# Optimization experiments

Hardware: AMD Instinct MI355X
Metric: run time of the kernel (lower is better)

## Reference

```python
import jax, jax.numpy as jnp
import numpy as np

B = 2          # point-cloud batches
N_PER_B = 8192 # non-empty pillars per batch
C = 128        # channels
H = 4          # heads
K = 4096       # max_tokens (top-k cap)
LN_EPS = 1e-5


def setup_inputs() -> dict:
    key = jax.random.key(0)
    ks = jax.random.split(key, 6)
    N = B * N_PER_B
    feats = jax.random.normal(ks[0], (N, C), dtype=jnp.float32)
    # equal-sized contiguous batch groups (sorted batch ids)
    batch_idx = jnp.repeat(jnp.arange(B, dtype=jnp.int64), N_PER_B)
    in_proj_w = jax.random.normal(ks[1], (3 * C, C), dtype=jnp.float32) * 0.02
    in_proj_b = jax.random.normal(ks[2], (3 * C,), dtype=jnp.float32) * 0.02
    out_proj_w = jax.random.normal(ks[3], (C, C), dtype=jnp.float32) * 0.02
    out_proj_b = jax.random.normal(ks[4], (C,), dtype=jnp.float32) * 0.02
    ln_w = jnp.ones((C,), dtype=jnp.float32)
    ln_b = jnp.zeros((C,), dtype=jnp.float32)
    return {"feats": feats, "batch_idx": batch_idx, "in_proj_w": in_proj_w,
            "in_proj_b": in_proj_b, "out_proj_w": out_proj_w,
            "out_proj_b": out_proj_b, "ln_w": ln_w, "ln_b": ln_b}


def _sparse_pillar_attn(feats, in_proj_w, in_proj_b, out_proj_w, out_proj_b, ln_w, ln_b):
    Dh = C // H
    x = feats.reshape(B, N_PER_B, C)
    # top-K tokens per batch by L2 feature norm (cap at max_tokens)
    norms = jnp.linalg.norm(x, axis=-1)                      # [B, n]
    _, topk = jax.lax.top_k(norms, K)                        # [B, K]
    xa = jnp.take_along_axis(x, topk[..., None], axis=1)     # [B, K, C]
    # MultiheadAttention (batch_first, self-attn)
    qkv = xa @ in_proj_w.T + in_proj_b                       # [B, K, 3C]
    q, k, v = jnp.split(qkv, 3, axis=-1)
    def heads(t):  # [B, K, C] -> [B, H, K, Dh]
        return t.reshape(B, K, H, Dh).transpose(0, 2, 1, 3)
    q, k, v = heads(q), heads(k), heads(v)
    scores = jnp.einsum('bhqd,bhkd->bhqk', q, k) / jnp.sqrt(jnp.float32(Dh))
    attn = jax.nn.softmax(scores, axis=-1)
    o = jnp.einsum('bhqk,bhkd->bhqd', attn, v)               # [B, H, K, Dh]
    o = o.transpose(0, 2, 1, 3).reshape(B, K, C)
    o = o @ out_proj_w.T + out_proj_b
    # residual + LayerNorm (dropout p=0 -> identity)
    h = xa + o
    mu = jnp.mean(h, axis=-1, keepdims=True)
    var = jnp.mean(jnp.square(h - mu), axis=-1, keepdims=True)
    y = (h - mu) / jnp.sqrt(var + LN_EPS) * ln_w + ln_b      # [B, K, C]
    # scatter back; non-selected tokens unchanged
    gidx = (jnp.arange(B)[:, None] * N_PER_B + topk).reshape(-1)
    return feats.at[gidx].set(y.reshape(-1, C))


def reference(feats, batch_idx, in_proj_w, in_proj_b, out_proj_w, out_proj_b, ln_w, ln_b):
    # batch_idx is sorted with equal group sizes, so groups are contiguous
    return _sparse_pillar_attn(feats, in_proj_w, in_proj_b, out_proj_w, out_proj_b, ln_w, ln_b)
```

## Files before the change

kernel.cpp:

```cpp
#include <hip/hip_runtime.h>
#include <hip/hip_bf16.h>
#include <stdint.h>

#define NPB 8192
#define CB 2
#define CC 128
#define HH 4
#define KTOK 4096
#define DH 32
#define NTOK (CB*KTOK)
#define K2C 0.25503402f

typedef __attribute__((ext_vector_type(8))) short sh8;
typedef __attribute__((ext_vector_type(4))) float fx4;
typedef __attribute__((ext_vector_type(16))) float fx16;
typedef __attribute__((ext_vector_type(2))) uint32_t ux2;
typedef __attribute__((ext_vector_type(4))) uint32_t ux4;

__device__ inline uint16_t f2bf(float f){
  uint32_t x = __float_as_uint(f);
  return (uint16_t)((x + 0x7FFFu + ((x>>16)&1u)) >> 16);
}
__device__ inline uint32_t pk2(float a, float b){
  return (uint32_t)f2bf(a) | ((uint32_t)f2bf(b) << 16);
}
__device__ inline float fast_exp2(float x){
#if __has_builtin(__builtin_amdgcn_exp2f)
  return __builtin_amdgcn_exp2f(x);
#else
  return exp2f(x);
#endif
}
__device__ inline uint32_t cvtpk1(float a, float b){
  uint32_t u;
  asm("v_cvt_pk_bf16_f32 %0, %1, %2" : "=v"(u) : "v"(a), "v"(b));
  return u;
}
__device__ inline void plswap(uint32_t& a, uint32_t& b){
#if __has_builtin(__builtin_amdgcn_permlane32_swap)
  typedef __attribute__((ext_vector_type(2))) unsigned int u2;
  u2 r = __builtin_amdgcn_permlane32_swap(a, b, false, false);
  a = r.x; b = r.y;
#else
  int hi = (threadIdx.x & 63) >> 5;
  uint32_t t = __shfl_xor(hi ? a : b, 32);
  uint32_t na = hi ? t : a;
  uint32_t nb = hi ? b : t;
  a = na; b = nb;
#endif
}
__device__ inline fx4 mfma32(sh8 a, sh8 b, fx4 c){
  return __builtin_amdgcn_mfma_f32_16x16x32_bf16(a, b, c, 0, 0, 0);
}
__device__ inline fx16 mfma32x32(sh8 a, sh8 b, fx16 c){
  return __builtin_amdgcn_mfma_f32_32x32x16_bf16(a, b, c, 0, 0, 0);
}
__device__ inline void gload_lds(const uint16_t* g, uint16_t* l){
  __builtin_amdgcn_global_load_lds(
      (const __attribute__((address_space(1))) uint32_t*)g,
      (__attribute__((address_space(3))) uint32_t*)l,
      16, 0, 0);
}

__global__ __launch_bounds__(256) void k_cpnw(const float* __restrict__ feats,
                                              float* __restrict__ out,
                                              uint32_t* __restrict__ keys,
                                              const float* __restrict__ wq,
                                              const float* __restrict__ wo,
                                              uint16_t* __restrict__ wqb,
                                              uint16_t* __restrict__ wob){
  int bx = blockIdx.x;
  if (bx < 1024){
    int wv = threadIdx.x >> 6, lane = threadIdx.x & 63;
    int row0 = bx*16 + wv*4;
#pragma unroll
    for (int r = 0; r < 4; ++r){
      int row = row0 + r;
      float2 v = *(const float2*)(feats + row*CC + lane*2);
      *(float2*)(out + row*CC + lane*2) = v;
      float s = v.x*v.x + v.y*v.y;
      for (int m = 1; m < 64; m <<= 1) s += __shfl_xor(s, m);
      if (lane == 0) keys[row] = __float_as_uint(s);
    }
  } else {
    int i = (bx - 1024)*256 + threadIdx.x;
    if (i < 3*CC*CC) wqb[i] = f2bf(wq[i]);
    else { int j = i - 3*CC*CC; wob[j] = f2bf(wo[j]); }
  }
}

__global__ __launch_bounds__(1024) void k_select(const uint32_t* __restrict__ keys,
                                                 int* __restrict__ sel){
  __shared__ uint32_t ka[NPB];
  __shared__ uint32_t hist[16*257];
  __shared__ uint32_t sh_prefix, sh_r;
  __shared__ int wsum[17];
  int tid = threadIdx.x, batch = blockIdx.x;
  int wv16 = tid >> 6;
  for (int i = tid; i < NPB; i += 1024) ka[i] = keys[batch*NPB + i];
  if (tid == 0){ sh_prefix = 0u; sh_r = KTOK; }
  __syncthreads();
  for (int pass = 0; pass < 4; ++pass){
    int shift = 24 - 8*pass;
    for (int i = tid; i < 16*257; i += 1024) hist[i] = 0u;
    __syncthreads();
    uint32_t pref = sh_prefix;
    uint32_t r0   = sh_r;
    uint32_t mask = (pass == 0) ? 0u : (0xFFFFFFFFu << (shift + 8));
    uint32_t* myh = &hist[wv16*257];
    for (int e = 0; e < 8; ++e){
      uint32_t k = ka[tid*8 + e];
      if ((k & mask) == pref) atomicAdd(&myh[(k >> shift) & 255], 1u);
    }
    __syncthreads();
    if (tid < 64){
      int lane = tid;
      uint32_t h0v = 0, h1v = 0, h2v = 0, h3v = 0;
      int b0 = lane*4;
#pragma unroll
      for (int w = 0; w < 16; ++w){
        const uint32_t* hw = &hist[w*257 + b0];
        h0v += hw[0]; h1v += hw[1]; h2v += hw[2]; h3v += hw[3];
      }
      uint32_t s3 = h3v, s2 = h2v + s3, s1 = h1v + s2, s0 = h0v + s1;
      uint32_t incl = s0;
      for (int d = 1; d < 64; d <<= 1){
        uint32_t t = __shfl_down(incl, d);
        if (lane + d < 64) incl += t;
      }
      uint32_t exA = incl - s0;
      uint32_t sfx[4] = {s0, s1, s2, s3};
      uint32_t hh[4]  = {h0v, h1v, h2v, h3v};
#pragma unroll
      for (int k = 0; k < 4; ++k){
        uint32_t inc_b = exA + sfx[k];
        uint32_t Sx    = inc_b - hh[k];
        if (Sx < r0 && inc_b >= r0){
          sh_prefix = pref | ((uint32_t)(b0 + k) << shift);
          sh_r = r0 - Sx;
        }
      }
    }
    __syncthreads();
  }
  uint32_t T = sh_prefix; int need = (int)sh_r;
  int lgt = 0, leq = 0;
  for (int e = 0; e < 8; ++e){
    uint32_t k = ka[tid*8 + e];
    lgt += (k > T); leq += (k == T);
  }
  int lane = tid & 63, wv = tid >> 6;
  int egt, tgt, eeq;
  {
    __syncthreads();
    int incl = lgt;
    for (int d = 1; d < 64; d <<= 1){ int t = __shfl_up(incl, d); if (lane >= d) incl += t; }
    if (lane == 63) wsum[wv] = incl;
    __syncthreads();
    if (tid == 0){ int run = 0; for (int w = 0; w < 16; ++w){ int t = wsum[w]; wsum[w] = run; run += t; } wsum[16] = run; }
    __syncthreads();
    egt = wsum[wv] + incl - lgt; tgt = wsum[16];
  }
  {
    __syncthreads();
    int incl = leq;
    for (int d = 1; d < 64; d <<= 1){ int t = __shfl_up(incl, d); if (lane >= d) incl += t; }
    if (lane == 63) wsum[wv] = incl;
    __syncthreads();
    if (tid == 0){ int run = 0; for (int w = 0; w < 16; ++w){ int t = wsum[w]; wsum[w] = run; run += t; } }
    __syncthreads();
    eeq = wsum[wv] + incl - leq;
  }
  int chi = tgt, gpos = egt, epos = eeq;
  for (int e = 0; e < 8; ++e){
    int i = tid*8 + e;
    uint32_t k = ka[i];
    if (k > T){ sel[batch*KTOK + (gpos++)] = batch*NPB + i; }
    else if (k == T){ if (epos < need) sel[batch*KTOK + chi + epos] = batch*NPB + i; epos++; }
  }
}

__global__ __launch_bounds__(256) void k_qkv(const float* __restrict__ feats,
                                             const int* __restrict__ sel,
                                             const uint16_t* __restrict__ wqb,
                                             const float* __restrict__ bias,
                                             uint16_t* __restrict__ Qg,
                                             uint16_t* __restrict__ Kg,
                                             uint16_t* __restrict__ Vt){
  int wave = threadIdx.x >> 6, lane = threadIdx.x & 63;
  int l15 = lane & 15, g = lane >> 4;
  int rt = blockIdx.x;
  int arow = rt*16 + l15;
  int grow = sel[arow];
  sh8 aF[4];
#pragma unroll
  for (int kk = 0; kk < 4; ++kk){
    const float* src = feats + grow*CC + kk*32 + g*8;
    float4 v0 = *(const float4*)(src);
    float4 v1 = *(const float4*)(src + 4);
    ux4 u;
    u.x = cvtpk1(v0.x, v0.y);
    u.y = cvtpk1(v0.z, v0.w);
    u.z = cvtpk1(v1.x, v1.y);
    u.w = cvtpk1(v1.z, v1.w);
    aF[kk] = *(sh8*)&u;
  }
  int tbase = rt*16;
  int b  = tbase >> 12;
  int q0 = (tbase & 4095) + g*4;
#pragma unroll
  for (int cg = 0; cg < 6; ++cg){
    int bcol = (cg*4 + wave)*16 + l15;
    fx4 acc = {0.f,0.f,0.f,0.f};
#pragma unroll
    for (int kk = 0; kk < 4; ++kk){
      sh8 bF = *(const sh8*)(wqb + bcol*CC + kk*32 + g*8);
      acc = mfma32(aF[kk], bF, acc);
    }
    int j = bcol;
    float bj = bias[j];
    if (j < CC){
      int h = j >> 5, d = j & 31;
      uint16_t* p = Qg + ((b*HH + h)*KTOK + q0)*DH + d;
#pragma unroll
      for (int i = 0; i < 4; ++i) p[i*DH] = f2bf((acc[i] + bj) * K2C);
    } else if (j < 2*CC){
      int jj = j - CC; int h = jj >> 5, d = jj & 31;
      uint16_t* p = Kg + ((b*HH + h)*KTOK + q0)*DH + d;
#pragma unroll
      for (int i = 0; i < 4; ++i) p[i*DH] = f2bf(acc[i] + bj);
    } else {
      int jj = j - 2*CC; int h = jj >> 5, d = jj & 31;
      uint16_t* p = Vt + ((b*HH + h)*DH + d)*KTOK + q0;
      ux2 w; w.x = pk2(acc[0]+bj, acc[1]+bj); w.y = pk2(acc[2]+bj, acc[3]+bj);
      *(ux2*)p = w;
    }
  }
}

__global__ __launch_bounds__(1024) void k_attn(const uint16_t* __restrict__ Qg,
                                               const uint16_t* __restrict__ Kg,
                                               const uint16_t* __restrict__ Vtg,
                                               uint16_t* __restrict__ O){
  __shared__ __align__(16) char lds[68096];
  int tid = threadIdx.x;
  int wv = tid >> 6, lane = tid & 63;
  int l31 = lane & 31, hi = lane >> 5;
  int seg = wv & 3, tq = wv >> 2;
  int bh = blockIdx.y;
  int qt = blockIdx.x;
  const uint16_t* Qp = Qg  + bh*KTOK*DH;
  const uint16_t* Kp = Kg  + bh*KTOK*DH;
  const uint16_t* Vp = Vtg + bh*DH*KTOK;
  int q = qt*128 + tq*32 + l31;
  sh8 qF0 = *(const sh8*)(Qp + q*DH + hi*8);
  sh8 qF1 = *(const sh8*)(Qp + q*DH + 16 + hi*8);

  uint16_t* st = (uint16_t*)lds;
  int key0 = seg*1024;
  int r16 = lane >> 2;
  int sx  = ((lane & 3) ^ ((r16 >> 1) & 3)) * 8;
  int sseg = wv & 3;
  int skey0 = sseg*1024;

  if (wv < 4){
    const uint16_t* kg = Kp + skey0*DH;
    uint16_t* d = st + sseg*4096;
#pragma unroll
    for (int ks = 0; ks < 2; ++ks){
      gload_lds(kg + (ks*32 + r16)*DH + sx,      d + ks*1024 + 0);
      gload_lds(kg + (ks*32 + 16 + r16)*DH + sx, d + ks*1024 + 512);
    }
  } else if (wv < 8){
    const uint16_t* vg = Vp + skey0;
    uint16_t* d = st + sseg*4096 + 2048;
#pragma unroll
    for (int ks = 0; ks < 2; ++ks){
      gload_lds(vg + r16*KTOK + ks*32 + sx,        d + ks*1024 + 0);
      gload_lds(vg + (16+r16)*KTOK + ks*32 + sx,   d + ks*1024 + 512);
    }
  }
  asm volatile("s_waitcnt vmcnt(0)" ::: "memory");
  __syncthreads();

  fx16 acc = {0,0,0,0,0,0,0,0,0,0,0,0,0,0,0,0};
  const fx16 z16 = {0,0,0,0,0,0,0,0,0,0,0,0,0,0,0,0};
  float lsum = 0.f;
  int swz = (l31 >> 1) & 3;
  int koff0 = l31*32 + ((hi     ^ swz)*8);
  int koff1 = l31*32 + (((hi+2) ^ swz)*8);

  for (int t = 0; t < 16; ++t){
    int b = t & 1;
    if (t < 15){
      int nk = skey0 + (t+1)*64;
      if (wv < 4){
        const uint16_t* kg = Kp + nk*DH;
        uint16_t* d = st + ((b^1)*4 + sseg)*4096;
#pragma unroll
        for (int ks = 0; ks < 2; ++ks){
          gload_lds(kg + (ks*32 + r16)*DH + sx,      d + ks*1024 + 0);
          gload_lds(kg + (ks*32 + 16 + r16)*DH + sx, d + ks*1024 + 512);
        }
      } else if (wv < 8){
        const uint16_t* vg = Vp + nk;
        uint16_t* d = st + ((b^1)*4 + sseg)*4096 + 2048;
#pragma unroll
        for (int ks = 0; ks < 2; ++ks){
          gload_lds(vg + r16*KTOK + ks*32 + sx,        d + ks*1024 + 0);
          gload_lds(vg + (16+r16)*KTOK + ks*32 + sx,   d + ks*1024 + 512);
        }
      }
    }
    const uint16_t* base = st + (b*4 + seg)*4096;
#pragma unroll
    for (int ks = 0; ks < 2; ++ks){
      const uint16_t* bK = base + ks*1024;
      const uint16_t* bV = base + 2048 + ks*1024;
      sh8 kA0 = *(const sh8*)(bK + koff0);
      sh8 kA1 = *(const sh8*)(bK + koff1);
      fx16 S = mfma32x32(kA0, qF0, z16);
      S = mfma32x32(kA1, qF1, S);
      float e[16];
#pragma unroll
      for (int r = 0; r < 16; ++r) e[r] = fast_exp2(S[r]);
      float ls = 0.f;
#pragma unroll
      for (int r = 0; r < 16; ++r) ls += e[r];
      lsum += ls;
      uint32_t X0 = cvtpk1(e[0], e[1]),   X1 = cvtpk1(e[2], e[3]);
      uint32_t X2 = cvtpk1(e[4], e[5]),   X3 = cvtpk1(e[6], e[7]);
      uint32_t X4 = cvtpk1(e[8], e[9]),   X5 = cvtpk1(e[10], e[11]);
      uint32_t X6 = cvtpk1(e[12], e[13]), X7 = cvtpk1(e[14], e[15]);
      plswap(X0, X2); plswap(X1, X3);
      plswap(X4, X6); plswap(X5, X7);
      ux4 w0, w1;
      w0.x = X0; w0.y = X1; w0.z = X2; w0.w = X3;
      w1.x = X4; w1.y = X5; w1.z = X6; w1.w = X7;
      sh8 pa0 = *(sh8*)&w0;
      sh8 pa1 = *(sh8*)&w1;
      sh8 vB0 = *(const sh8*)(bV + koff0);
      sh8 vB1 = *(const sh8*)(bV + koff1);
      acc = mfma32x32(pa0, vB0, acc);
      acc = mfma32x32(pa1, vB1, acc);
    }
    asm volatile("s_waitcnt vmcnt(0)" ::: "memory");
    __syncthreads();
  }

  float* cmb = (float*)lds;
  float* lwp = (float*)(lds + 65536);
  float* ltr = (float*)(lds + 65536 + 2048);
  lsum += __shfl_xor(lsum, 32);
#pragma unroll
  for (int i = 0; i < 16; i += 4){
    fx4 p = {acc[i], acc[i+1], acc[i+2], acc[i+3]};
    *(fx4*)&cmb[((tq*4 + seg)*64 + lane)*16 + i] = p;
  }
  if (!hi) lwp[wv*32 + l31] = lsum;
  __syncthreads();
  if (seg == 0){
#pragma unroll
    for (int s = 1; s < 4; ++s){
#pragma unroll
      for (int i = 0; i < 16; i += 4){
        fx4 p = *(const fx4*)&cmb[((tq*4 + s)*64 + lane)*16 + i];
        acc[i] += p.x; acc[i+1] += p.y; acc[i+2] += p.z; acc[i+3] += p.w;
      }
    }
    float lt = (lwp[(tq*4+0)*32 + l31] + lwp[(tq*4+1)*32 + l31])
             + (lwp[(tq*4+2)*32 + l31] + lwp[(tq*4+3)*32 + l31]);
    if (!hi) ltr[tq*32 + l31] = lt;
    fx4 La = *(const fx4*)&ltr[tq*32 + 4*hi];
    fx4 Lb = *(const fx4*)&ltr[tq*32 + 8 + 4*hi];
    fx4 Lc = *(const fx4*)&ltr[tq*32 + 16 + 4*hi];
    fx4 Ld = *(const fx4*)&ltr[tq*32 + 24 + 4*hi];
    fx4 Ra = {1.f/La.x, 1.f/La.y, 1.f/La.z, 1.f/La.w};
    fx4 Rb = {1.f/Lb.x, 1.f/Lb.y, 1.f/Lb.z, 1.f/Lb.w};
    fx4 Rc = {1.f/Lc.x, 1.f/Lc.y, 1.f/Lc.z, 1.f/Lc.w};
    fx4 Rd = {1.f/Ld.x, 1.f/Ld.y, 1.f/Ld.z, 1.f/Ld.w};
    int bb = bh >> 2, h = bh & 3;
    uint16_t* op = O + (bb*KTOK + qt*128 + tq*32)*CC + h*DH + l31;
#pragma unroll
    for (int r = 0; r < 16; ++r){
      int qd = (r&3) + 8*(r>>2) + 4*hi;
      float rv = (r<4) ? Ra[r&3] : (r<8) ? Rb[r&3] : (r<12) ? Rc[r&3] : Rd[r&3];
      op[qd*CC] = f2bf(acc[r] * rv);
    }
  }
}

__global__ __launch_bounds__(256) void k_outln(const uint16_t* __restrict__ O,
                                               const uint16_t* __restrict__ wob,
                                               const float* __restrict__ bo,
                                               const float* __restrict__ feats,
                                               const int* __restrict__ sel,
                                               const float* __restrict__ lnw,
                                               const float* __restrict__ lnb,
                                               float* __restrict__ out){
  __shared__ float red[16][4][2];
  int wave = threadIdx.x >> 6, lane = threadIdx.x & 63;
  int l15 = lane & 15, g = lane >> 4;
  int rt = blockIdx.x;
  int arow = rt*16 + l15;
  int jA = wave*32 + l15, jB = jA + 16;
  fx4 accA = {0,0,0,0}, accB = {0,0,0,0};
#pragma unroll
  for (int kk = 0; kk < 4; ++kk){
    sh8 aF = *(const sh8*)(O   + arow*CC + kk*32 + g*8);
    sh8 b0 = *(const sh8*)(wob + jA*CC   + kk*32 + g*8);
    sh8 b1 = *(const sh8*)(wob + jB*CC   + kk*32 + g*8);
    accA = mfma32(aF, b0, accA);
    accB = mfma32(aF, b1, accB);
  }
  float bjA = bo[jA], bjB = bo[jB];
  float hA[4], hB[4]; int gl[4];
#pragma unroll
  for (int i = 0; i < 4; ++i){
    int r = rt*16 + g*4 + i;
    int grow = sel[r];
    gl[i] = grow;
    hA[i] = accA[i] + bjA + feats[grow*CC + jA];
    hB[i] = accB[i] + bjB + feats[grow*CC + jB];
  }
#pragma unroll
  for (int i = 0; i < 4; ++i){
    float s  = hA[i] + hB[i];
    float s2 = hA[i]*hA[i] + hB[i]*hB[i];
    for (int mk = 1; mk < 16; mk <<= 1){ s += __shfl_xor(s, mk); s2 += __shfl_xor(s2, mk); }
    if (l15 == 0){ red[g*4+i][wave][0] = s; red[g*4+i][wave][1] = s2; }
  }
  __syncthreads();
  float w0 = lnw[jA], w1 = lnw[jB], b0v = lnb[jA], b1v = lnb[jB];
#pragma unroll
  for (int i = 0; i < 4; ++i){
    int rl = g*4 + i;
    float tot  = red[rl][0][0] + red[rl][1][0] + red[rl][2][0] + red[rl][3][0];
    float tot2 = red[rl][0][1] + red[rl][1][1] + red[rl][2][1] + red[rl][3][1];
    float mu  = tot  * (1.f/128.f);
    float var = tot2 * (1.f/128.f) - mu*mu;
    float rs = rsqrtf(var + 1e-5f);
    out[gl[i]*CC + jA] = (hA[i]-mu)*rs*w0 + b0v;
    out[gl[i]*CC + jB] = (hB[i]-mu)*rs*w1 + b1v;
  }
}

extern "C" void kernel_launch(void* const* d_in, const int* in_sizes, int n_in,
                              void* d_out, int out_size, void* d_ws, size_t ws_size,
                              hipStream_t stream){
  const float* feats = (const float*)d_in[0];
  const float* wqkv  = (const float*)d_in[2];
  const float* bqkv  = (const float*)d_in[3];
  const float* wout  = (const float*)d_in[4];
  const float* bout  = (const float*)d_in[5];
  const float* lnw   = (const float*)d_in[6];
  const float* lnb   = (const float*)d_in[7];
  float* out = (float*)d_out;
  char* ws = (char*)d_ws;

  uint32_t* keys = (uint32_t*)(ws + 0);
  int*      sel  = (int*)     (ws + 65536);
  uint16_t* wqb  = (uint16_t*)(ws + 98304);
  uint16_t* wob  = (uint16_t*)(ws + 196608);
  uint16_t* Qg   = (uint16_t*)(ws + 2326528);
  uint16_t* Kg   = (uint16_t*)(ws + 4423680);
  uint16_t* Vt   = (uint16_t*)(ws + 6520832);
  uint16_t* O    = (uint16_t*)(ws + 8617984);

  hipLaunchKernelGGL(k_cpnw,   dim3(1280),   dim3(256),  0, stream,
                     feats, out, keys, wqkv, wout, wqb, wob);
  hipLaunchKernelGGL(k_select, dim3(2),      dim3(1024), 0, stream, keys, sel);
  hipLaunchKernelGGL(k_qkv,    dim3(512),    dim3(256),  0, stream,
                     feats, sel, wqb, bqkv, Qg, Kg, Vt);
  hipLaunchKernelGGL(k_attn,   dim3(32,8),   dim3(1024), 0, stream, Qg, Kg, Vt, O);
  hipLaunchKernelGGL(k_outln,  dim3(512),    dim3(256),  0, stream, O, wob, bout, feats, sel, lnw, lnb, out);
}
```

Before: 72.21 us.

## Triple-buffer K/V staging in attention kernel with partial vmcnt waits

Replaces the double-buffered K/V LDS staging with a three-slot ring that prefetches two tiles ahead. Each iteration waits only for the oldest outstanding loads (vmcnt(4)) before a raw s_barrier, so global-to-LDS loads for the next two tiles can overlap compute instead of being drained to zero each step. LDS use grows to 96KB per block, which may limit occupancy, though a 1024-thread block was likely already one per CU.

```diff
diff --git a/kernel.cpp b/kernel.cpp
--- a/kernel.cpp
+++ b/kernel.cpp
@@ -242,7 +242,7 @@
                                                const uint16_t* __restrict__ Kg,
                                                const uint16_t* __restrict__ Vtg,
                                                uint16_t* __restrict__ O){
-  __shared__ __align__(16) char lds[68096];
+  __shared__ __align__(16) char lds[98304];
   int tid = threadIdx.x;
   int wv = tid >> 6, lane = tid & 63;
   int l31 = lane & 31, hi = lane >> 5;
@@ -257,31 +257,33 @@
   sh8 qF1 = *(const sh8*)(Qp + q*DH + 16 + hi*8);
 
   uint16_t* st = (uint16_t*)lds;
-  int key0 = seg*1024;
   int r16 = lane >> 2;
   int sx  = ((lane & 3) ^ ((r16 >> 1) & 3)) * 8;
   int sseg = wv & 3;
   int skey0 = sseg*1024;
 
-  if (wv < 4){
-    const uint16_t* kg = Kp + skey0*DH;
-    uint16_t* d = st + sseg*4096;
-#pragma unroll
-    for (int ks = 0; ks < 2; ++ks){
-      gload_lds(kg + (ks*32 + r16)*DH + sx,      d + ks*1024 + 0);
-      gload_lds(kg + (ks*32 + 16 + r16)*DH + sx, d + ks*1024 + 512);
-    }
-  } else if (wv < 8){
-    const uint16_t* vg = Vp + skey0;
-    uint16_t* d = st + sseg*4096 + 2048;
-#pragma unroll
-    for (int ks = 0; ks < 2; ++ks){
-      gload_lds(vg + r16*KTOK + ks*32 + sx,        d + ks*1024 + 0);
-      gload_lds(vg + (16+r16)*KTOK + ks*32 + sx,   d + ks*1024 + 512);
-    }
-  }
-  asm volatile("s_waitcnt vmcnt(0)" ::: "memory");
-  __syncthreads();
+  auto STAGE = [&](int c, int bi){
+    if (wv < 4){
+      const uint16_t* kg = Kp + (skey0 + c*64)*DH;
+      uint16_t* d = st + (bi*4 + sseg)*4096;
+#pragma unroll
+      for (int ks = 0; ks < 2; ++ks){
+        gload_lds(kg + (ks*32 + r16)*DH + sx,      d + ks*1024 + 0);
+        gload_lds(kg + (ks*32 + 16 + r16)*DH + sx, d + ks*1024 + 512);
+      }
+    } else if (wv < 8){
+      const uint16_t* vg = Vp + skey0 + c*64;
+      uint16_t* d = st + (bi*4 + sseg)*4096 + 2048;
+#pragma unroll
+      for (int ks = 0; ks < 2; ++ks){
+        gload_lds(vg + r16*KTOK + ks*32 + sx,        d + ks*1024 + 0);
+        gload_lds(vg + (16+r16)*KTOK + ks*32 + sx,   d + ks*1024 + 512);
+      }
+    }
+  };
+
+  STAGE(0, 0);
+  STAGE(1, 1);
 
   fx16 acc = {0,0,0,0,0,0,0,0,0,0,0,0,0,0,0,0};
   const fx16 z16 = {0,0,0,0,0,0,0,0,0,0,0,0,0,0,0,0};
@@ -290,29 +292,17 @@
   int koff0 = l31*32 + ((hi     ^ swz)*8);
   int koff1 = l31*32 + (((hi+2) ^ swz)*8);
 
+  int bi = 0;
   for (int t = 0; t < 16; ++t){
-    int b = t & 1;
-    if (t < 15){
-      int nk = skey0 + (t+1)*64;
-      if (wv < 4){
-        const uint16_t* kg = Kp + nk*DH;
-        uint16_t* d = st + ((b^1)*4 + sseg)*4096;
-#pragma unroll
-        for (int ks = 0; ks < 2; ++ks){
-          gload_lds(kg + (ks*32 + r16)*DH + sx,      d + ks*1024 + 0);
-          gload_lds(kg + (ks*32 + 16 + r16)*DH + sx, d + ks*1024 + 512);
-        }
-      } else if (wv < 8){
-        const uint16_t* vg = Vp + nk;
-        uint16_t* d = st + ((b^1)*4 + sseg)*4096 + 2048;
-#pragma unroll
-        for (int ks = 0; ks < 2; ++ks){
-          gload_lds(vg + r16*KTOK + ks*32 + sx,        d + ks*1024 + 0);
-          gload_lds(vg + (16+r16)*KTOK + ks*32 + sx,   d + ks*1024 + 512);
-        }
-      }
-    }
-    const uint16_t* base = st + (b*4 + seg)*4096;
+    if (t < 15) asm volatile("s_waitcnt vmcnt(4)" ::: "memory");
+    else        asm volatile("s_waitcnt vmcnt(0)" ::: "memory");
+    asm volatile("s_barrier" ::: "memory");
+    __builtin_amdgcn_sched_barrier(0);
+    if (t + 2 < 16){
+      int nbi = bi + 2; if (nbi >= 3) nbi -= 3;
+      STAGE(t + 2, nbi);
+    }
+    const uint16_t* base = st + (bi*4 + seg)*4096;
 #pragma unroll
     for (int ks = 0; ks < 2; ++ks){
       const uint16_t* bK = base + ks*1024;
@@ -344,10 +334,10 @@
       acc = mfma32x32(pa0, vB0, acc);
       acc = mfma32x32(pa1, vB1, acc);
     }
-    asm volatile("s_waitcnt vmcnt(0)" ::: "memory");
-    __syncthreads();
-  }
-
+    ++bi; if (bi >= 3) bi = 0;
+  }
+
+  __syncthreads();
   float* cmb = (float*)lds;
   float* lwp = (float*)(lds + 65536);
   float* ltr = (float*)(lds + 65536 + 2048);
```

New measurement: 73.14 us. About the same (+1.3%).

## Compute softmax row sums via MFMA with ones and remove permlane swaps

Applied to the files above, without the earlier changes.

Drops the per-lane scalar exp summation and the permlane32 swaps used to rearrange P for the PV MFMA. It permutes the K row order during the LDS staging load so the S accumulator layout can be fed straight into the PV MFMA. Row sums now come from two extra MFMAs of P against a ones vector, moving VALU work onto the matrix units. The cost is doubling the MFMA count in the PV stage plus another 16-register accumulator, and the scattered write of row sums must match the new layout.

```diff
diff --git a/kernel.cpp b/kernel.cpp
--- a/kernel.cpp
+++ b/kernel.cpp
@@ -35,19 +35,6 @@
   uint32_t u;
   asm("v_cvt_pk_bf16_f32 %0, %1, %2" : "=v"(u) : "v"(a), "v"(b));
   return u;
-}
-__device__ inline void plswap(uint32_t& a, uint32_t& b){
-#if __has_builtin(__builtin_amdgcn_permlane32_swap)
-  typedef __attribute__((ext_vector_type(2))) unsigned int u2;
-  u2 r = __builtin_amdgcn_permlane32_swap(a, b, false, false);
-  a = r.x; b = r.y;
-#else
-  int hi = (threadIdx.x & 63) >> 5;
-  uint32_t t = __shfl_xor(hi ? a : b, 32);
-  uint32_t na = hi ? t : a;
-  uint32_t nb = hi ? b : t;
-  a = na; b = nb;
-#endif
 }
 __device__ inline fx4 mfma32(sh8 a, sh8 b, fx4 c){
   return __builtin_amdgcn_mfma_f32_16x16x32_bf16(a, b, c, 0, 0, 0);
@@ -257,8 +244,8 @@
   sh8 qF1 = *(const sh8*)(Qp + q*DH + 16 + hi*8);
 
   uint16_t* st = (uint16_t*)lds;
-  int key0 = seg*1024;
   int r16 = lane >> 2;
+  int kr  = (r16 & 3) | ((r16 & 4) << 1) | ((r16 & 8) >> 1);
   int sx  = ((lane & 3) ^ ((r16 >> 1) & 3)) * 8;
   int sseg = wv & 3;
   int skey0 = sseg*1024;
@@ -268,8 +255,8 @@
     uint16_t* d = st + sseg*4096;
 #pragma unroll
     for (int ks = 0; ks < 2; ++ks){
-      gload_lds(kg + (ks*32 + r16)*DH + sx,      d + ks*1024 + 0);
-      gload_lds(kg + (ks*32 + 16 + r16)*DH + sx, d + ks*1024 + 512);
+      gload_lds(kg + (ks*32 + kr)*DH + sx,      d + ks*1024 + 0);
+      gload_lds(kg + (ks*32 + 16 + kr)*DH + sx, d + ks*1024 + 512);
     }
   } else if (wv < 8){
     const uint16_t* vg = Vp + skey0;
@@ -283,9 +270,11 @@
   asm volatile("s_waitcnt vmcnt(0)" ::: "memory");
   __syncthreads();
 
-  fx16 acc = {0,0,0,0,0,0,0,0,0,0,0,0,0,0,0,0};
+  fx16 acc  = {0,0,0,0,0,0,0,0,0,0,0,0,0,0,0,0};
+  fx16 accl = {0,0,0,0,0,0,0,0,0,0,0,0,0,0,0,0};
   const fx16 z16 = {0,0,0,0,0,0,0,0,0,0,0,0,0,0,0,0};
-  float lsum = 0.f;
+  const short ONEB = (short)0x3F80;
+  sh8 onesB = {ONEB,ONEB,ONEB,ONEB,ONEB,ONEB,ONEB,ONEB};
   int swz = (l31 >> 1) & 3;
   int koff0 = l31*32 + ((hi     ^ swz)*8);
   int koff1 = l31*32 + (((hi+2) ^ swz)*8);
@@ -299,8 +288,8 @@
         uint16_t* d = st + ((b^1)*4 + sseg)*4096;
 #pragma unroll
         for (int ks = 0; ks < 2; ++ks){
-          gload_lds(kg + (ks*32 + r16)*DH + sx,      d + ks*1024 + 0);
-          gload_lds(kg + (ks*32 + 16 + r16)*DH + sx, d + ks*1024 + 512);
+          gload_lds(kg + (ks*32 + kr)*DH + sx,      d + ks*1024 + 0);
+          gload_lds(kg + (ks*32 + 16 + kr)*DH + sx, d + ks*1024 + 512);
         }
       } else if (wv < 8){
         const uint16_t* vg = Vp + nk;
@@ -324,25 +313,19 @@
       float e[16];
 #pragma unroll
       for (int r = 0; r < 16; ++r) e[r] = fast_exp2(S[r]);
-      float ls = 0.f;
-#pragma unroll
-      for (int r = 0; r < 16; ++r) ls += e[r];
-      lsum += ls;
-      uint32_t X0 = cvtpk1(e[0], e[1]),   X1 = cvtpk1(e[2], e[3]);
-      uint32_t X2 = cvtpk1(e[4], e[5]),   X3 = cvtpk1(e[6], e[7]);
-      uint32_t X4 = cvtpk1(e[8], e[9]),   X5 = cvtpk1(e[10], e[11]);
-      uint32_t X6 = cvtpk1(e[12], e[13]), X7 = cvtpk1(e[14], e[15]);
-      plswap(X0, X2); plswap(X1, X3);
-      plswap(X4, X6); plswap(X5, X7);
       ux4 w0, w1;
-      w0.x = X0; w0.y = X1; w0.z = X2; w0.w = X3;
-      w1.x = X4; w1.y = X5; w1.z = X6; w1.w = X7;
+      w0.x = cvtpk1(e[0],  e[1]);  w0.y = cvtpk1(e[2],  e[3]);
+      w0.z = cvtpk1(e[4],  e[5]);  w0.w = cvtpk1(e[6],  e[7]);
+      w1.x = cvtpk1(e[8],  e[9]);  w1.y = cvtpk1(e[10], e[11]);
+      w1.z = cvtpk1(e[12], e[13]); w1.w = cvtpk1(e[14], e[15]);
       sh8 pa0 = *(sh8*)&w0;
       sh8 pa1 = *(sh8*)&w1;
       sh8 vB0 = *(const sh8*)(bV + koff0);
       sh8 vB1 = *(const sh8*)(bV + koff1);
-      acc = mfma32x32(pa0, vB0, acc);
-      acc = mfma32x32(pa1, vB1, acc);
+      acc  = mfma32x32(pa0, vB0, acc);
+      acc  = mfma32x32(pa1, vB1, acc);
+      accl = mfma32x32(pa0, onesB, accl);
+      accl = mfma32x32(pa1, onesB, accl);
     }
     asm volatile("s_waitcnt vmcnt(0)" ::: "memory");
     __syncthreads();
@@ -351,13 +334,16 @@
   float* cmb = (float*)lds;
   float* lwp = (float*)(lds + 65536);
   float* ltr = (float*)(lds + 65536 + 2048);
-  lsum += __shfl_xor(lsum, 32);
 #pragma unroll
   for (int i = 0; i < 16; i += 4){
     fx4 p = {acc[i], acc[i+1], acc[i+2], acc[i+3]};
     *(fx4*)&cmb[((tq*4 + seg)*64 + lane)*16 + i] = p;
   }
-  if (!hi) lwp[wv*32 + l31] = lsum;
+  if (l31 == 0){
+#pragma unroll
+    for (int r = 0; r < 16; ++r)
+      lwp[wv*32 + (r&3) + 8*(r>>2) + 4*hi] = accl[r];
+  }
   __syncthreads();
   if (seg == 0){
 #pragma unroll
```

Result: no change. 71.02 us (-1.6%).
